# Optimization experiments

Hardware: AMD Instinct MI355X
Metric: run time of the kernel (lower is better)

The kernel has to match this reference:

```python
import jax, jax.numpy as jnp
import numpy as np

V, E, H = 50257, 256, 512
B, S = 4, 512


def setup_inputs() -> dict:
    key = jax.random.key(0)
    ks = jax.random.split(key, 16)
    k_ih = 1.0 / np.sqrt(H)
    inp = {
        "input_ids": jax.random.randint(ks[0], (B, S), 0, V, dtype=jnp.int64) if jax.config.jax_enable_x64 else jax.random.randint(ks[0], (B, S), 0, V, dtype=jnp.int32),
        "embedding": jax.random.normal(ks[1], (V, E), jnp.float32) * 0.02,
        "W_ih": jax.random.uniform(ks[2], (3 * H, E), jnp.float32, -k_ih, k_ih),
        "W_hh": jax.random.uniform(ks[3], (3 * H, H), jnp.float32, -k_ih, k_ih),
        "b_ih": jax.random.uniform(ks[4], (3 * H,), jnp.float32, -k_ih, k_ih),
        "b_hh": jax.random.uniform(ks[5], (3 * H,), jnp.float32, -k_ih, k_ih),
        "W_he": jax.random.normal(ks[6], (E, H), jnp.float32) * 0.02,
        "b_he": jnp.zeros((E,), jnp.float32),
        "output_bias": jnp.zeros((V,), jnp.float32),
        "W_read": jax.random.normal(ks[7], (1, H), jnp.float32) * 0.02,
        "b_read": jnp.zeros((1,), jnp.float32),
        "W_write": jax.random.normal(ks[8], (1, H), jnp.float32) * 0.02,
        "b_write": jnp.zeros((1,), jnp.float32),
        "W_decay": jax.random.normal(ks[9], (1, H), jnp.float32) * 0.02,
        "b_decay": jnp.zeros((1,), jnp.float32),
        "memory_scale": jnp.asarray(4.0, jnp.float32),
    }
    return inp


def _gru(x, W_ih, W_hh, b_ih, b_hh):
    # x: [B,S,E] -> states [B,S,H], PyTorch GRU gate order (r, z, n)
    xg = jnp.einsum("bse,ge->bsg", x, W_ih) + b_ih  # [B,S,3H]

    def step(h, xg_t):
        hg = h @ W_hh.T + b_hh
        xr, xz, xn = jnp.split(xg_t, 3, axis=-1)
        hr, hz, hn = jnp.split(hg, 3, axis=-1)
        r = jax.nn.sigmoid(xr + hr)
        z = jax.nn.sigmoid(xz + hz)
        n = jnp.tanh(xn + r * hn)
        h_new = (1.0 - z) * n + z * h
        return h_new, h_new

    h0 = jnp.zeros((x.shape[0], W_hh.shape[1]), x.dtype)
    _, states = jax.lax.scan(step, h0, jnp.swapaxes(xg, 0, 1))
    return jnp.swapaxes(states, 0, 1)  # [B,S,H]


def reference(input_ids, embedding, W_ih, W_hh, b_ih, b_hh, W_he, b_he,
              output_bias, W_read, b_read, W_write, b_write, W_decay, b_decay,
              memory_scale):
    emb = embedding[input_ids]                      # [B,S,E]
    states = _gru(emb, W_ih, W_hh, b_ih, b_hh)      # [B,S,H]
    proj = jnp.einsum("bsh,eh->bse", states, W_he) + b_he
    base = jnp.einsum("bse,ve->bsv", proj, embedding) + output_bias  # [B,S,V]

    read = jax.nn.sigmoid(jnp.einsum("bsh,oh->bso", states, W_read) + b_read) * memory_scale
    decay = jax.nn.sigmoid(jnp.einsum("bsh,oh->bso", states, W_decay) + b_decay)
    write = jax.nn.sigmoid(jnp.einsum("bsh,oh->bso", states, W_write) + b_write)

    bsz = base.shape[0]
    rows = jnp.arange(bsz)

    def step(m, xs):
        base_t, read_t, decay_t, write_t, ids_t = xs
        out = base_t + read_t * m                   # read before write
        m = m * decay_t
        m = m.at[rows, ids_t].add(write_t[:, 0])
        return m, out

    xs = (jnp.swapaxes(base, 0, 1), jnp.swapaxes(read, 0, 1),
          jnp.swapaxes(decay, 0, 1), jnp.swapaxes(write, 0, 1),
          jnp.swapaxes(input_ids, 0, 1))
    m0 = jnp.zeros((bsz, base.shape[2]), base.dtype)
    _, outs = jax.lax.scan(step, m0, xs)            # [S,B,V]
    return jnp.swapaxes(outs, 0, 1)                 # [B,S,V]
```

## Files before the change

kernel.cpp:

```cpp
#include <hip/hip_runtime.h>
#include <hip/hip_bf16.h>
#include <hip/hip_fp16.h>
#include <math.h>

#define V_SIZE 50257
#define V_PAD  50304
#define E_DIM  256
#define H_DIM  512
#define G_DIM  1536
#define B_SZ   4
#define S_LEN  512

typedef __attribute__((ext_vector_type(8))) short bf16x8;
typedef __attribute__((ext_vector_type(4))) float f32x4;
typedef __attribute__((ext_vector_type(2))) _Float16 h16x2;

__device__ __forceinline__ float bf2f(unsigned short u) {
  union { unsigned int i; float f; } x; x.i = ((unsigned int)u) << 16; return x.f;
}
__device__ __forceinline__ unsigned short f2bf(float f) {
  __hip_bfloat16 h = __float2bfloat16(f);
  return reinterpret_cast<unsigned short&>(h);
}
__device__ __forceinline__ float sigmoidf_(float x) { return 1.0f / (1.0f + expf(-x)); }
__device__ __forceinline__ float fsig(float x) { return 1.0f / (1.0f + __expf(-x)); }
__device__ __forceinline__ float ftanh(float x) { return 1.0f - 2.0f / (__expf(2.0f * x) + 1.0f); }

__device__ __forceinline__ h16x2 as_h2(unsigned int u) {
  union { unsigned int u; h16x2 h; } x; x.u = u; return x.h;
}

#if defined(__has_builtin)
#if __has_builtin(__builtin_amdgcn_fdot2)
#define HAVE_FDOT2 1
#endif
#endif
__device__ __forceinline__ float fdot2_(unsigned int a, unsigned int b, float c) {
#ifdef HAVE_FDOT2
  return __builtin_amdgcn_fdot2(as_h2(a), as_h2(b), c, false);
#else
  h16x2 ha = as_h2(a), hb = as_h2(b);
  return c + (float)ha[0] * (float)hb[0] + (float)ha[1] * (float)hb[1];
#endif
}

__device__ __forceinline__ void gload_lds16(const void* g, void* l) {
  __builtin_amdgcn_global_load_lds((const __attribute__((address_space(1))) unsigned int*)g,
                                   (__attribute__((address_space(3))) unsigned int*)l, 16, 0, 0);
}

__global__ __launch_bounds__(256) void k_emb2bf(const float* __restrict__ emb,
                                                __hip_bfloat16* __restrict__ out) {
  const long total = (long)V_PAD * E_DIM;
  for (long i = (long)blockIdx.x * 256 + threadIdx.x; i < total; i += (long)gridDim.x * 256) {
    int row = (int)(i >> 8);
    float v = (row < V_SIZE) ? emb[i] : 0.0f;
    out[i] = __float2bfloat16(v);
  }
}

__global__ __launch_bounds__(256) void k_xg(const int* __restrict__ ids, const float* __restrict__ emb,
                                            const float* __restrict__ W_ih, const float* __restrict__ b_ih,
                                            float* __restrict__ xg) {
  __shared__ float embs[16][260];
  __shared__ float wl[64][133];
  const int g0 = blockIdx.x * 128, n0 = blockIdx.y * 16, tid = threadIdx.x;
  for (int idx = tid; idx < 16 * 256; idx += 256) {
    int n = idx >> 8, e = idx & 255;
    embs[n][e] = emb[(long)ids[n0 + n] * E_DIM + e];
  }
  const int g = tid & 127, ng = tid >> 7;
  float acc[8] = {0.f,0.f,0.f,0.f,0.f,0.f,0.f,0.f};
  for (int e0 = 0; e0 < 256; e0 += 64) {
    __syncthreads();
    for (int idx = tid; idx < 128 * 64; idx += 256) {
      int r = idx >> 6, c = idx & 63;
      wl[c][r] = W_ih[(long)(g0 + r) * E_DIM + e0 + c];
    }
    __syncthreads();
    for (int c = 0; c < 64; ++c) {
      float w = wl[c][g];
      #pragma unroll
      for (int j = 0; j < 8; ++j) acc[j] += w * embs[ng * 8 + j][e0 + c];
    }
  }
  const float bias = b_ih[g0 + g];
  #pragma unroll
  for (int j = 0; j < 8; ++j) {
    int n = n0 + ng * 8 + j;
    xg[(long)n * G_DIM + g0 + g] = acc[j] + bias;
  }
}

#define NWG 32
#define WROWU 261
#define WPLU  (16 * WROWU)
#define HROWU 260
__global__ __launch_bounds__(512, 1) void k_scan(const float* __restrict__ xg,
                                                 const float* __restrict__ W_hh,
                                                 const float* __restrict__ b_hh,
                                                 float* __restrict__ states,
                                                 unsigned long long* __restrict__ h_hist) {
  __shared__ unsigned int Wp[3 * WPLU];
  __shared__ unsigned int hp[4 * HROWU];
  __shared__ float red[2][8][16][12];
  const int wg = blockIdx.x, tid = threadIdx.x;
  const int i0 = wg * 16;
  for (int e = tid; e < 3 * 16 * 256; e += 512) {
    int q = e >> 12, i = (e >> 8) & 15, p = e & 255;
    float2 w2 = reinterpret_cast<const float2*>(W_hh + (long)((q << 9) + i0 + i) * H_DIM)[p];
    unsigned int pk = (unsigned int)__half_as_ushort(__float2half(w2.x)) |
                      ((unsigned int)__half_as_ushort(__float2half(w2.y)) << 16);
    Wp[q * WPLU + i * WROWU + p] = pk;
  }
  const int wave = tid >> 6, l = tid & 63, il = l >> 2, part = l & 3;
  const int ii = tid >> 2, bb = tid & 3;
  const int pidx = tid >> 1;
  float h_prev = 0.0f;
  float bhr = 0.f, bhz = 0.f, bhn = 0.f;
  if (tid < 64) { bhr = b_hh[i0 + ii]; bhz = b_hh[512 + i0 + ii]; bhn = b_hh[1024 + i0 + ii]; }
  __syncthreads();

  for (int t = 0; t < S_LEN; ++t) {
    float xr_v = 0.f, xz_v = 0.f, xn_v = 0.f;
    if (tid < 64) {
      const float* xgrow = xg + (long)(bb * S_LEN + t) * G_DIM + i0 + ii;
      xr_v = xgrow[0]; xz_v = xgrow[512]; xn_v = xgrow[1024];
    }
    float acc[3][4] = {{0.f,0.f,0.f,0.f},{0.f,0.f,0.f,0.f},{0.f,0.f,0.f,0.f}};
    if (t > 0) {
      const unsigned long long* hb = h_hist + (long)(t - 1) * 512;
      unsigned long long v;
      do {
        v = __hip_atomic_load(hb + tid, __ATOMIC_RELAXED, __HIP_MEMORY_SCOPE_AGENT);
      } while (v == 0xFFFFFFFFFFFFFFFFull);
      const unsigned int lo = (unsigned int)v, hi = (unsigned int)(v >> 32);
      const unsigned int plo = __shfl_xor(lo, 1), phi = __shfl_xor(hi, 1);
      if ((tid & 1) == 0) {
        hp[pidx]         = (lo & 0xffffu) | (plo << 16);
        hp[HROWU + pidx] = (lo >> 16) | (phi & 0xffff0000u ? (plo & 0xffff0000u) : (plo & 0xffff0000u));
      } else {
        hp[2 * HROWU + pidx] = (phi & 0xffffu) | (hi << 16);
        hp[3 * HROWU + pidx] = (phi >> 16) | (hi & 0xffff0000u);
      }
      const int pbase = (wave << 5) + (part << 3);
      #pragma unroll
      for (int j = 0; j < 8; ++j) {
        const int p = pbase + j;
        const unsigned int w_r = Wp[il * WROWU + p];
        const unsigned int w_z = Wp[WPLU + il * WROWU + p];
        const unsigned int w_n = Wp[2 * WPLU + il * WROWU + p];
        const unsigned int h0 = hp[p];
        const unsigned int h1 = hp[HROWU + p];
        const unsigned int h2 = hp[2 * HROWU + p];
        const unsigned int h3 = hp[3 * HROWU + p];
        acc[0][0] = fdot2_(w_r, h0, acc[0][0]); acc[0][1] = fdot2_(w_r, h1, acc[0][1]);
        acc[0][2] = fdot2_(w_r, h2, acc[0][2]); acc[0][3] = fdot2_(w_r, h3, acc[0][3]);
        acc[1][0] = fdot2_(w_z, h0, acc[1][0]); acc[1][1] = fdot2_(w_z, h1, acc[1][1]);
        acc[1][2] = fdot2_(w_z, h2, acc[1][2]); acc[1][3] = fdot2_(w_z, h3, acc[1][3]);
        acc[2][0] = fdot2_(w_n, h0, acc[2][0]); acc[2][1] = fdot2_(w_n, h1, acc[2][1]);
        acc[2][2] = fdot2_(w_n, h2, acc[2][2]); acc[2][3] = fdot2_(w_n, h3, acc[2][3]);
      }
    }
    #pragma unroll
    for (int q = 0; q < 3; ++q)
      #pragma unroll
      for (int b = 0; b < 4; ++b) {
        float v = acc[q][b];
        v += __shfl_xor(v, 1);
        v += __shfl_xor(v, 2);
        if (part == 0) red[t & 1][wave][il][q * 4 + b] = v;
      }
    __syncthreads();
    if (tid < 64) {
      float hr = bhr, hz = bhz, hn = bhn;
      #pragma unroll
      for (int w = 0; w < 8; ++w) {
        hr += red[t & 1][w][ii][0 + bb];
        hz += red[t & 1][w][ii][4 + bb];
        hn += red[t & 1][w][ii][8 + bb];
      }
      float r  = fsig(xr_v + hr);
      float z  = fsig(xz_v + hz);
      float nn = ftanh(xn_v + r * hn);
      float h_new = (1.0f - z) * nn + z * h_prev;
      h_prev = h_new;
      unsigned int hu = (unsigned int)__half_as_ushort(__float2half(h_new));
      unsigned int v1 = __shfl_down(hu, 1);
      unsigned int v2 = __shfl_down(hu, 2);
      unsigned int v3 = __shfl_down(hu, 3);
      if (bb == 0) {
        unsigned long long pk = (unsigned long long)(hu | (v1 << 16)) |
                                ((unsigned long long)(v2 | (v3 << 16)) << 32);
        __hip_atomic_store(h_hist + (long)t * 512 + i0 + ii, pk,
                           __ATOMIC_RELAXED, __HIP_MEMORY_SCOPE_AGENT);
      }
      states[(long)(bb * S_LEN + t) * H_DIM + i0 + ii] = h_new;
    }
  }
}

__global__ __launch_bounds__(256) void k_gates(const float* __restrict__ states,
     const float* __restrict__ W_read, const float* __restrict__ b_read,
     const float* __restrict__ W_write, const float* __restrict__ b_write,
     const float* __restrict__ W_decay, const float* __restrict__ b_decay,
     const float* __restrict__ mscale,
     float* __restrict__ read_s, float* __restrict__ decay_s, float* __restrict__ write_s) {
  __shared__ float wr[512], ww[512], wd[512];
  const int tid = threadIdx.x;
  for (int i = tid; i < 512; i += 256) { wr[i] = W_read[i]; ww[i] = W_write[i]; wd[i] = W_decay[i]; }
  __syncthreads();
  const int wave = tid >> 6, l = tid & 63;
  const float br = b_read[0], bw = b_write[0], bd = b_decay[0], ms = mscale[0];
  for (int r = 0; r < 16; ++r) {
    const int n = blockIdx.x * 64 + wave * 16 + r;
    const float* st = states + (long)n * H_DIM;
    float ar = 0.f, aw = 0.f, ad = 0.f;
    #pragma unroll
    for (int h0 = 0; h0 < 512; h0 += 64) {
      float s = st[h0 + l];
      ar += s * wr[h0 + l]; aw += s * ww[h0 + l]; ad += s * wd[h0 + l];
    }
    #pragma unroll
    for (int k = 1; k < 64; k <<= 1) {
      ar += __shfl_xor(ar, k); aw += __shfl_xor(aw, k); ad += __shfl_xor(ad, k);
    }
    if (l == 0) {
      read_s[n]  = sigmoidf_(ar + br) * ms;
      write_s[n] = sigmoidf_(aw + bw);
      decay_s[n] = sigmoidf_(ad + bd);
    }
  }
}

__global__ __launch_bounds__(256) void k_proj(const float* __restrict__ states,
                                              const float* __restrict__ W_he,
                                              const float* __restrict__ b_he,
                                              __hip_bfloat16* __restrict__ proj) {
  __shared__ float sts[32][64];
  __shared__ float wle[64][69];
  const int n0 = blockIdx.x * 32, e0 = blockIdx.y * 64, tid = threadIdx.x;
  const int e = tid & 63, ng = tid >> 6;
  float acc[8] = {0.f,0.f,0.f,0.f,0.f,0.f,0.f,0.f};
  for (int h0 = 0; h0 < 512; h0 += 64) {
    __syncthreads();
    for (int idx = tid; idx < 32 * 64; idx += 256) {
      int n = idx >> 6, c = idx & 63;
      sts[n][c] = states[(long)(n0 + n) * H_DIM + h0 + c];
    }
    for (int idx = tid; idx < 64 * 64; idx += 256) {
      int r = idx >> 6, c = idx & 63;
      wle[c][r] = W_he[(long)(e0 + r) * H_DIM + h0 + c];
    }
    __syncthreads();
    for (int c = 0; c < 64; ++c) {
      float w = wle[c][e];
      #pragma unroll
      for (int j = 0; j < 8; ++j) acc[j] += w * sts[ng * 8 + j][c];
    }
  }
  const float bias = b_he[e0 + e];
  #pragma unroll
  for (int j = 0; j < 8; ++j) {
    int n = n0 + ng * 8 + j;
    proj[(long)n * E_DIM + e0 + e] = __float2bfloat16(acc[j] + bias);
  }
}

__global__ __launch_bounds__(256) void k_base(const __hip_bfloat16* __restrict__ A,
                                              const __hip_bfloat16* __restrict__ Bm,
                                              const float* __restrict__ obias,
                                              float* __restrict__ C) {
  __shared__ unsigned short As[128 * 32], Bs[128 * 32];
  const int n0 = blockIdx.x * 128, m0 = blockIdx.y * 128, tid = threadIdx.x;
  const int wid = tid >> 6, l = tid & 63;
  const int wm = wid >> 1, wn = wid & 1;
  f32x4 acc[4][4];
  #pragma unroll
  for (int mi = 0; mi < 4; ++mi)
    #pragma unroll
    for (int ni = 0; ni < 4; ++ni) acc[mi][ni] = (f32x4){0.f, 0.f, 0.f, 0.f};

  for (int kk = 0; kk < 256; kk += 32) {
    __syncthreads();
    #pragma unroll
    for (int s = 0; s < 2; ++s) {
      const int cibase = wid * 128 + s * 64;
      const int ci = cibase + l;
      const int row = ci >> 2, cq = ci & 3;
      gload_lds16(A + (long)(m0 + row) * E_DIM + kk + cq * 8, As + cibase * 8);
      gload_lds16(Bm + (long)(n0 + row) * E_DIM + kk + cq * 8, Bs + cibase * 8);
    }
    __syncthreads();
    bf16x8 af[4], bfr[4];
    const int krow = (l >> 4) * 8;
    #pragma unroll
    for (int mi = 0; mi < 4; ++mi) {
      int row = wm * 64 + mi * 16 + (l & 15);
      af[mi] = *reinterpret_cast<const bf16x8*>(&As[row * 32 + krow]);
    }
    #pragma unroll
    for (int ni = 0; ni < 4; ++ni) {
      int row = wn * 64 + ni * 16 + (l & 15);
      bfr[ni] = *reinterpret_cast<const bf16x8*>(&Bs[row * 32 + krow]);
    }
    #pragma unroll
    for (int mi = 0; mi < 4; ++mi)
      #pragma unroll
      for (int ni = 0; ni < 4; ++ni)
        acc[mi][ni] = __builtin_amdgcn_mfma_f32_16x16x32_bf16(af[mi], bfr[ni], acc[mi][ni], 0, 0, 0);
  }
  #pragma unroll
  for (int mi = 0; mi < 4; ++mi) {
    const int rowb = m0 + wm * 64 + mi * 16 + (l >> 4) * 4;
    #pragma unroll
    for (int ni = 0; ni < 4; ++ni) {
      const int col = n0 + wn * 64 + ni * 16 + (l & 15);
      if (col < V_SIZE) {
        const float ob = obias[col];
        #pragma unroll
        for (int r = 0; r < 4; ++r)
          C[(long)(rowb + r) * V_SIZE + col] = acc[mi][ni][r] + ob;
      }
    }
  }
}

__global__ __launch_bounds__(64) void k_corr(const int* __restrict__ ids,
                                             const float* __restrict__ read_s,
                                             const float* __restrict__ decay_s,
                                             const float* __restrict__ write_s,
                                             float* __restrict__ out) {
  __shared__ int ids_s[512];
  __shared__ float rd[512], dc[512], wrs[512];
  const int b = blockIdx.x, c = blockIdx.y, l = threadIdx.x;
  for (int t = l; t < 512; t += 64) {
    int n = b * 512 + t;
    ids_s[t] = ids[n]; rd[t] = read_s[n]; dc[t] = decay_s[n]; wrs[t] = write_s[n];
  }
  __syncthreads();
  const int j = c * 64 + l;
  const int v = ids_s[j];
  for (int jj = 0; jj < j; ++jj) if (ids_s[jj] == v) return;
  float m = wrs[j];
  float* outb = out + (long)b * S_LEN * V_SIZE + v;
  for (int t = j + 1; t < 512; ++t) {
    outb[(long)t * V_SIZE] += rd[t] * m;
    m *= dc[t];
    if (ids_s[t] == v) m += wrs[t];
  }
}

extern "C" void kernel_launch(void* const* d_in, const int* in_sizes, int n_in,
                              void* d_out, int out_size, void* d_ws, size_t ws_size,
                              hipStream_t stream) {
  const int*   ids     = (const int*)d_in[0];
  const float* emb     = (const float*)d_in[1];
  const float* W_ih    = (const float*)d_in[2];
  const float* W_hh    = (const float*)d_in[3];
  const float* b_ih    = (const float*)d_in[4];
  const float* b_hh    = (const float*)d_in[5];
  const float* W_he    = (const float*)d_in[6];
  const float* b_he    = (const float*)d_in[7];
  const float* obias   = (const float*)d_in[8];
  const float* W_read  = (const float*)d_in[9];
  const float* b_read  = (const float*)d_in[10];
  const float* W_write = (const float*)d_in[11];
  const float* b_write = (const float*)d_in[12];
  const float* W_decay = (const float*)d_in[13];
  const float* b_decay = (const float*)d_in[14];
  const float* mscale  = (const float*)d_in[15];

  char* ws = (char*)d_ws;
  __hip_bfloat16* emb_bf  = (__hip_bfloat16*)ws;
  __hip_bfloat16* proj_bf = (__hip_bfloat16*)(ws + 25755648);
  float* read_s  = (float*)(ws + 26804224);
  float* decay_s = (float*)(ws + 26812416);
  float* write_s = (float*)(ws + 26820608);

  char* ob = (char*)d_out;
  float* xg  = (float*)ob;
  float* states = (float*)(ob + 12582912);
  unsigned long long* h_hist = (unsigned long long*)(ob + 16777216);
  float* out = (float*)d_out;

  hipMemsetAsync(h_hist, 0xFF, (size_t)S_LEN * 512 * sizeof(unsigned long long), stream);
  k_emb2bf<<<2048, 256, 0, stream>>>(emb, emb_bf);
  dim3 gxg(12, 128);
  k_xg<<<gxg, 256, 0, stream>>>(ids, emb, W_ih, b_ih, xg);
  k_scan<<<NWG, 512, 0, stream>>>(xg, W_hh, b_hh, states, h_hist);
  k_gates<<<32, 256, 0, stream>>>(states, W_read, b_read, W_write, b_write, W_decay, b_decay,
                                  mscale, read_s, decay_s, write_s);
  dim3 gpj(64, 4);
  k_proj<<<gpj, 256, 0, stream>>>(states, W_he, b_he, proj_bf);
  dim3 gb(393, 16);
  k_base<<<gb, 256, 0, stream>>>(proj_bf, emb_bf, obias, out);
  dim3 gc(4, 8);
  k_corr<<<gc, 64, 0, stream>>>(ids, read_s, decay_s, write_s, out);
}
```

Measured before the change: 1.966 ms.

## Overlap embedding conversion with GRU scan, fuse proj/gates, swizzle GEMM, parallelize corr

The fp32-to-bf16 embedding conversion now runs inside extra blocks of the scan launch, so it can use the CUs left idle by the 32-block recurrent scan. The projection and gate kernels are merged into one launch. The base GEMM grid is flattened with a block-index swizzle, likely to improve cache reuse. The correction kernel now runs one block per position, with a single-lane serial recurrence and a parallel scatter of the output updates. The risks are that the extra blocks take LDS and occupancy alongside the scan, and that the serial lane-0 loop in k_corr lengthens each block.

```diff
diff --git a/kernel.cpp b/kernel.cpp
--- a/kernel.cpp
+++ b/kernel.cpp
@@ -15,13 +15,6 @@
 typedef __attribute__((ext_vector_type(4))) float f32x4;
 typedef __attribute__((ext_vector_type(2))) _Float16 h16x2;
 
-__device__ __forceinline__ float bf2f(unsigned short u) {
-  union { unsigned int i; float f; } x; x.i = ((unsigned int)u) << 16; return x.f;
-}
-__device__ __forceinline__ unsigned short f2bf(float f) {
-  __hip_bfloat16 h = __float2bfloat16(f);
-  return reinterpret_cast<unsigned short&>(h);
-}
 __device__ __forceinline__ float sigmoidf_(float x) { return 1.0f / (1.0f + expf(-x)); }
 __device__ __forceinline__ float fsig(float x) { return 1.0f / (1.0f + __expf(-x)); }
 __device__ __forceinline__ float ftanh(float x) { return 1.0f - 2.0f / (__expf(2.0f * x) + 1.0f); }
@@ -29,7 +22,6 @@
 __device__ __forceinline__ h16x2 as_h2(unsigned int u) {
   union { unsigned int u; h16x2 h; } x; x.u = u; return x.h;
 }
-
 #if defined(__has_builtin)
 #if __has_builtin(__builtin_amdgcn_fdot2)
 #define HAVE_FDOT2 1
@@ -43,20 +35,9 @@
   return c + (float)ha[0] * (float)hb[0] + (float)ha[1] * (float)hb[1];
 #endif
 }
-
 __device__ __forceinline__ void gload_lds16(const void* g, void* l) {
   __builtin_amdgcn_global_load_lds((const __attribute__((address_space(1))) unsigned int*)g,
                                    (__attribute__((address_space(3))) unsigned int*)l, 16, 0, 0);
-}
-
-__global__ __launch_bounds__(256) void k_emb2bf(const float* __restrict__ emb,
-                                                __hip_bfloat16* __restrict__ out) {
-  const long total = (long)V_PAD * E_DIM;
-  for (long i = (long)blockIdx.x * 256 + threadIdx.x; i < total; i += (long)gridDim.x * 256) {
-    int row = (int)(i >> 8);
-    float v = (row < V_SIZE) ? emb[i] : 0.0f;
-    out[i] = __float2bfloat16(v);
-  }
 }
 
 __global__ __launch_bounds__(256) void k_xg(const int* __restrict__ ids, const float* __restrict__ emb,
@@ -93,6 +74,7 @@
 }
 
 #define NWG 32
+#define NEXTRA 216
 #define WROWU 261
 #define WPLU  (16 * WROWU)
 #define HROWU 260
@@ -100,11 +82,25 @@
                                                  const float* __restrict__ W_hh,
                                                  const float* __restrict__ b_hh,
                                                  float* __restrict__ states,
-                                                 unsigned long long* __restrict__ h_hist) {
+                                                 unsigned long long* __restrict__ h_hist,
+                                                 const float* __restrict__ emb,
+                                                 __hip_bfloat16* __restrict__ emb_bf) {
   __shared__ unsigned int Wp[3 * WPLU];
   __shared__ unsigned int hp[4 * HROWU];
   __shared__ float red[2][8][16][12];
-  const int wg = blockIdx.x, tid = threadIdx.x;
+  const int bid = blockIdx.x, tid = threadIdx.x;
+
+  if (bid >= NWG) {
+    const long total = (long)V_PAD * E_DIM;
+    for (long i = (long)(bid - NWG) * 512 + tid; i < total; i += (long)NEXTRA * 512) {
+      int row = (int)(i >> 8);
+      float v = (row < V_SIZE) ? emb[i] : 0.0f;
+      emb_bf[i] = __float2bfloat16(v);
+    }
+    return;
+  }
+
+  const int wg = bid;
   const int i0 = wg * 16;
   for (int e = tid; e < 3 * 16 * 256; e += 512) {
     int q = e >> 12, i = (e >> 8) & 15, p = e & 255;
@@ -138,7 +134,7 @@
       const unsigned int plo = __shfl_xor(lo, 1), phi = __shfl_xor(hi, 1);
       if ((tid & 1) == 0) {
         hp[pidx]         = (lo & 0xffffu) | (plo << 16);
-        hp[HROWU + pidx] = (lo >> 16) | (phi & 0xffff0000u ? (plo & 0xffff0000u) : (plo & 0xffff0000u));
+        hp[HROWU + pidx] = (lo >> 16) | (plo & 0xffff0000u);
       } else {
         hp[2 * HROWU + pidx] = (phi & 0xffffu) | (hi << 16);
         hp[3 * HROWU + pidx] = (phi >> 16) | (hi & 0xffff0000u);
@@ -200,70 +196,70 @@
   }
 }
 
-__global__ __launch_bounds__(256) void k_gates(const float* __restrict__ states,
+__global__ __launch_bounds__(256) void k_projgates(const float* __restrict__ states,
+     const float* __restrict__ W_he, const float* __restrict__ b_he,
+     __hip_bfloat16* __restrict__ proj,
      const float* __restrict__ W_read, const float* __restrict__ b_read,
      const float* __restrict__ W_write, const float* __restrict__ b_write,
      const float* __restrict__ W_decay, const float* __restrict__ b_decay,
      const float* __restrict__ mscale,
      float* __restrict__ read_s, float* __restrict__ decay_s, float* __restrict__ write_s) {
-  __shared__ float wr[512], ww[512], wd[512];
-  const int tid = threadIdx.x;
-  for (int i = tid; i < 512; i += 256) { wr[i] = W_read[i]; ww[i] = W_write[i]; wd[i] = W_decay[i]; }
-  __syncthreads();
-  const int wave = tid >> 6, l = tid & 63;
-  const float br = b_read[0], bw = b_write[0], bd = b_decay[0], ms = mscale[0];
-  for (int r = 0; r < 16; ++r) {
-    const int n = blockIdx.x * 64 + wave * 16 + r;
-    const float* st = states + (long)n * H_DIM;
-    float ar = 0.f, aw = 0.f, ad = 0.f;
-    #pragma unroll
+  __shared__ float sm[6464];
+  const int bid = blockIdx.x, tid = threadIdx.x;
+  if (bid < 256) {
+    float* sts = sm;
+    float* wle = sm + 2048;
+    const int n0 = (bid & 63) * 32, e0 = (bid >> 6) * 64;
+    const int e = tid & 63, ng = tid >> 6;
+    float acc[8] = {0.f,0.f,0.f,0.f,0.f,0.f,0.f,0.f};
     for (int h0 = 0; h0 < 512; h0 += 64) {
-      float s = st[h0 + l];
-      ar += s * wr[h0 + l]; aw += s * ww[h0 + l]; ad += s * wd[h0 + l];
-    }
-    #pragma unroll
-    for (int k = 1; k < 64; k <<= 1) {
-      ar += __shfl_xor(ar, k); aw += __shfl_xor(aw, k); ad += __shfl_xor(ad, k);
-    }
-    if (l == 0) {
-      read_s[n]  = sigmoidf_(ar + br) * ms;
-      write_s[n] = sigmoidf_(aw + bw);
-      decay_s[n] = sigmoidf_(ad + bd);
-    }
-  }
-}
-
-__global__ __launch_bounds__(256) void k_proj(const float* __restrict__ states,
-                                              const float* __restrict__ W_he,
-                                              const float* __restrict__ b_he,
-                                              __hip_bfloat16* __restrict__ proj) {
-  __shared__ float sts[32][64];
-  __shared__ float wle[64][69];
-  const int n0 = blockIdx.x * 32, e0 = blockIdx.y * 64, tid = threadIdx.x;
-  const int e = tid & 63, ng = tid >> 6;
-  float acc[8] = {0.f,0.f,0.f,0.f,0.f,0.f,0.f,0.f};
-  for (int h0 = 0; h0 < 512; h0 += 64) {
-    __syncthreads();
-    for (int idx = tid; idx < 32 * 64; idx += 256) {
-      int n = idx >> 6, c = idx & 63;
-      sts[n][c] = states[(long)(n0 + n) * H_DIM + h0 + c];
-    }
-    for (int idx = tid; idx < 64 * 64; idx += 256) {
-      int r = idx >> 6, c = idx & 63;
-      wle[c][r] = W_he[(long)(e0 + r) * H_DIM + h0 + c];
-    }
-    __syncthreads();
-    for (int c = 0; c < 64; ++c) {
-      float w = wle[c][e];
-      #pragma unroll
-      for (int j = 0; j < 8; ++j) acc[j] += w * sts[ng * 8 + j][c];
-    }
-  }
-  const float bias = b_he[e0 + e];
-  #pragma unroll
-  for (int j = 0; j < 8; ++j) {
-    int n = n0 + ng * 8 + j;
-    proj[(long)n * E_DIM + e0 + e] = __float2bfloat16(acc[j] + bias);
+      __syncthreads();
+      for (int idx = tid; idx < 32 * 64; idx += 256) {
+        int n = idx >> 6, c = idx & 63;
+        sts[n * 64 + c] = states[(long)(n0 + n) * H_DIM + h0 + c];
+      }
+      for (int idx = tid; idx < 64 * 64; idx += 256) {
+        int r = idx >> 6, c = idx & 63;
+        wle[c * 69 + r] = W_he[(long)(e0 + r) * H_DIM + h0 + c];
+      }
+      __syncthreads();
+      for (int c = 0; c < 64; ++c) {
+        float w = wle[c * 69 + e];
+        #pragma unroll
+        for (int j = 0; j < 8; ++j) acc[j] += w * sts[(ng * 8 + j) * 64 + c];
+      }
+    }
+    const float bias = b_he[e0 + e];
+    #pragma unroll
+    for (int j = 0; j < 8; ++j) {
+      int n = n0 + ng * 8 + j;
+      proj[(long)n * E_DIM + e0 + e] = __float2bfloat16(acc[j] + bias);
+    }
+  } else {
+    float* wr = sm; float* ww = sm + 512; float* wd = sm + 1024;
+    for (int i = tid; i < 512; i += 256) { wr[i] = W_read[i]; ww[i] = W_write[i]; wd[i] = W_decay[i]; }
+    __syncthreads();
+    const int wave = tid >> 6, l = tid & 63;
+    const float br = b_read[0], bw = b_write[0], bd = b_decay[0], ms = mscale[0];
+    for (int r = 0; r < 16; ++r) {
+      const int n = (bid - 256) * 64 + wave * 16 + r;
+      const float* st = states + (long)n * H_DIM;
+      float ar = 0.f, aw = 0.f, ad = 0.f;
+      #pragma unroll
+      for (int h0 = 0; h0 < 512; h0 += 64) {
+        float s = st[h0 + l];
+        ar += s * wr[h0 + l]; aw += s * ww[h0 + l]; ad += s * wd[h0 + l];
+      }
+      #pragma unroll
+      for (int k = 1; k < 64; k <<= 1) {
+        ar += __shfl_xor(ar, k); aw += __shfl_xor(aw, k); ad += __shfl_xor(ad, k);
+      }
+      if (l == 0) {
+        read_s[n]  = sigmoidf_(ar + br) * ms;
+        write_s[n] = sigmoidf_(aw + bw);
+        decay_s[n] = sigmoidf_(ad + bd);
+      }
+    }
   }
 }
 
@@ -272,7 +268,9 @@
                                               const float* __restrict__ obias,
                                               float* __restrict__ C) {
   __shared__ unsigned short As[128 * 32], Bs[128 * 32];
-  const int n0 = blockIdx.x * 128, m0 = blockIdx.y * 128, tid = threadIdx.x;
+  const int swz = (blockIdx.x & 7) * 786 + (blockIdx.x >> 3);
+  const int m0 = (swz & 15) * 128, n0 = (swz >> 4) * 128;
+  const int tid = threadIdx.x;
   const int wid = tid >> 6, l = tid & 63;
   const int wm = wid >> 1, wn = wid & 1;
   f32x4 acc[4][4];
@@ -332,23 +330,29 @@
                                              const float* __restrict__ write_s,
                                              float* __restrict__ out) {
   __shared__ int ids_s[512];
-  __shared__ float rd[512], dc[512], wrs[512];
-  const int b = blockIdx.x, c = blockIdx.y, l = threadIdx.x;
+  __shared__ float rd[512], dc[512], wrs[512], c[512];
+  const int b = blockIdx.x, j = blockIdx.y, l = threadIdx.x;
   for (int t = l; t < 512; t += 64) {
     int n = b * 512 + t;
     ids_s[t] = ids[n]; rd[t] = read_s[n]; dc[t] = decay_s[n]; wrs[t] = write_s[n];
   }
   __syncthreads();
-  const int j = c * 64 + l;
   const int v = ids_s[j];
-  for (int jj = 0; jj < j; ++jj) if (ids_s[jj] == v) return;
-  float m = wrs[j];
+  bool own = true;
+  for (int jj = l; jj < j; jj += 64) if (ids_s[jj] == v) own = false;
+  if (!__all(own)) return;
+  if (l == 0) {
+    float m = wrs[j];
+    for (int t = j + 1; t < 512; ++t) {
+      c[t] = rd[t] * m;
+      m *= dc[t];
+      if (ids_s[t] == v) m += wrs[t];
+    }
+  }
+  __syncthreads();
   float* outb = out + (long)b * S_LEN * V_SIZE + v;
-  for (int t = j + 1; t < 512; ++t) {
-    outb[(long)t * V_SIZE] += rd[t] * m;
-    m *= dc[t];
-    if (ids_s[t] == v) m += wrs[t];
-  }
+  for (int t = j + 1 + l; t < 512; t += 64)
+    outb[(long)t * V_SIZE] += c[t];
 }
 
 extern "C" void kernel_launch(void* const* d_in, const int* in_sizes, int n_in,
@@ -379,22 +383,19 @@
   float* write_s = (float*)(ws + 26820608);
 
   char* ob = (char*)d_out;
-  float* xg  = (float*)ob;
+  float* xg     = (float*)ob;
   float* states = (float*)(ob + 12582912);
   unsigned long long* h_hist = (unsigned long long*)(ob + 16777216);
   float* out = (float*)d_out;
 
   hipMemsetAsync(h_hist, 0xFF, (size_t)S_LEN * 512 * sizeof(unsigned long long), stream);
-  k_emb2bf<<<2048, 256, 0, stream>>>(emb, emb_bf);
   dim3 gxg(12, 128);
   k_xg<<<gxg, 256, 0, stream>>>(ids, emb, W_ih, b_ih, xg);
-  k_scan<<<NWG, 512, 0, stream>>>(xg, W_hh, b_hh, states, h_hist);
-  k_gates<<<32, 256, 0, stream>>>(states, W_read, b_read, W_write, b_write, W_decay, b_decay,
-                                  mscale, read_s, decay_s, write_s);
-  dim3 gpj(64, 4);
-  k_proj<<<gpj, 256, 0, stream>>>(states, W_he, b_he, proj_bf);
-  dim3 gb(393, 16);
-  k_base<<<gb, 256, 0, stream>>>(proj_bf, emb_bf, obias, out);
-  dim3 gc(4, 8);
+  k_scan<<<NWG + NEXTRA, 512, 0, stream>>>(xg, W_hh, b_hh, states, h_hist, emb, emb_bf);
+  k_projgates<<<288, 256, 0, stream>>>(states, W_he, b_he, proj_bf,
+                                       W_read, b_read, W_write, b_write, W_decay, b_decay,
+                                       mscale, read_s, decay_s, write_s);
+  k_base<<<6288, 256, 0, stream>>>(proj_bf, emb_bf, obias, out);
+  dim3 gc(4, 512);
   k_corr<<<gc, 64, 0, stream>>>(ids, read_s, decay_s, write_s, out);
 }
```

Result: faster. 1.645 ms, median of 3 (-16.3%).
